# Kernel optimization log

Hardware: AMD Instinct MI355X
Metric: run time of the kernel (lower is better)

The kernel has to match this reference:

```python
import jax, jax.numpy as jnp
import numpy as np

B, L, D, DEG = 32, 1024, 512, 8
E = B * L * DEG  # 262144 edges total
N = B * L


def setup_inputs() -> dict:
    key = jax.random.key(0)
    ks = jax.random.split(key, 8)
    text_feature = jax.random.normal(ks[0], (B, L, D), jnp.float32)
    # edge list per sample (torch.nonzero(edge_matrix[i]) equivalent), offset by b*L like PyG batching
    src_local = jax.random.randint(ks[1], (E,), 0, L, jnp.int32)
    dst_local = jax.random.randint(ks[2], (E,), 0, L, jnp.int32)
    boff = (jnp.arange(E, dtype=jnp.int32) // (E // B)) * L
    edge_src = src_local + boff
    edge_dst = dst_local + boff
    s = 1.0 / np.sqrt(D)
    W1 = jax.random.uniform(ks[3], (D, D), jnp.float32, -s, s)   # node Linear
    b1 = jax.random.uniform(ks[4], (D,), jnp.float32, -s, s)
    gamma = jnp.ones((D,), jnp.float32)      # BatchNorm1d weight
    beta = jnp.zeros((D,), jnp.float32)      # BatchNorm1d bias
    run_mean = jnp.zeros((D,), jnp.float32)  # BN running stats (eval mode)
    run_var = jnp.ones((D,), jnp.float32)
    alpha1 = jnp.array(0.25, jnp.float32)    # PReLU (node MLP)
    Wg = jax.random.uniform(ks[5], (D, D), jnp.float32, -s, s)   # GCNConv lin (bias=False)
    bg = jnp.zeros((D,), jnp.float32)        # GCNConv bias
    alpha2 = jnp.array(0.25, jnp.float32)    # PReLU (after GCN)
    return {"text_feature": text_feature, "edge_src": edge_src, "edge_dst": edge_dst,
            "W1": W1, "b1": b1, "gamma": gamma, "beta": beta,
            "run_mean": run_mean, "run_var": run_var, "alpha1": alpha1,
            "Wg": Wg, "bg": bg, "alpha2": alpha2}


def reference(text_feature, edge_src, edge_dst, W1, b1, gamma, beta,
              run_mean, run_var, alpha1, Wg, bg, alpha2):
    Bs, Ls, Ds = text_feature.shape
    Nn = Bs * Ls
    xf = text_feature.reshape(Nn, Ds)
    # node MLP: Linear -> BatchNorm1d (eval) -> PReLU
    h = xf @ W1 + b1
    h = (h - run_mean) * jax.lax.rsqrt(run_var + 1e-5) * gamma + beta
    h = jnp.where(h >= 0, h, alpha1 * h)
    # GCNConv: add self loops, symmetric degree norm, gather->scatter-add, + bias
    nodes = jnp.arange(Nn, dtype=edge_src.dtype)
    src = jnp.concatenate([edge_src, nodes])
    dst = jnp.concatenate([edge_dst, nodes])
    deg = jnp.zeros((Nn,), h.dtype).at[dst].add(1.0)  # in-degree incl. self loop, >= 1
    dinv = jax.lax.rsqrt(deg)
    xw = h @ Wg                               # [N, D]
    msg = (xw * dinv[:, None])[src]           # gather D^{-1/2}-scaled messages [E+N, D]
    agg = jnp.zeros_like(xw).at[dst].add(msg) * dinv[:, None]
    g = agg + bg
    g = jnp.where(g >= 0, g, alpha2 * g)      # PReLU
    g = g.reshape(Bs, Ls, Ds)
    # F.normalize(p=2, dim=2) + residual (original input)
    g = g / jnp.clip(jnp.linalg.norm(g, axis=2, keepdims=True), 1e-12)
    return g + text_feature
```

## Files before the change

kernel.cpp:

```cpp
#include <hip/hip_runtime.h>
#include <math.h>

#define DD    512
#define NN    32768
#define EE    262144

typedef float f32x4 __attribute__((ext_vector_type(4)));
typedef __bf16 bf16x8 __attribute__((ext_vector_type(8)));

#define AS1 __attribute__((address_space(1)))
#define AS3 __attribute__((address_space(3)))

__global__ void k_zero(int* __restrict__ cnt) {
    int i = blockIdx.x * 256 + threadIdx.x;
    if (i < NN) cnt[i] = 0;
}

__global__ void k_count(const int* __restrict__ dst, int* __restrict__ cnt) {
    int e = blockIdx.x * 256 + threadIdx.x;
    if (e < EE) atomicAdd(&cnt[dst[e]], 1);
}

__global__ __launch_bounds__(1024) void k_scan(
    const int* __restrict__ cnt, int* __restrict__ offs,
    int* __restrict__ cursor, float* __restrict__ dinv)
{
    __shared__ int part[1024];
    int t = threadIdx.x;
    int base = t * 32;
    int local[32];
    int s = 0;
#pragma unroll
    for (int i = 0; i < 32; ++i) { local[i] = s; s += cnt[base + i]; }
    part[t] = s;
    __syncthreads();
    for (int off = 1; off < 1024; off <<= 1) {
        int v = (t >= off) ? part[t - off] : 0;
        __syncthreads();
        part[t] += v;
        __syncthreads();
    }
    int prev = (t == 0) ? 0 : part[t - 1];
#pragma unroll
    for (int i = 0; i < 32; ++i) {
        int o = prev + local[i];
        offs[base + i] = o;
        cursor[base + i] = o;
        dinv[base + i] = rsqrtf((float)cnt[base + i] + 1.0f);
    }
    if (t == 1023) offs[NN] = part[1023];
}

__global__ void k_fill(const int* __restrict__ src, const int* __restrict__ dst,
                       int* __restrict__ cursor, int* __restrict__ csr) {
    int e = blockIdx.x * 256 + threadIdx.x;
    if (e < EE) {
        int d = dst[e];
        int p = atomicAdd(&cursor[d], 1);
        csr[p] = src[e];
    }
}

__global__ __launch_bounds__(256) void k_wt(const float* __restrict__ W1, const float* __restrict__ Wg,
                                            __bf16* __restrict__ W1t, __bf16* __restrict__ Wgt) {
    __shared__ float tile[32][33];
    const float* W = blockIdx.z ? Wg : W1;
    __bf16* Wt = blockIdx.z ? Wgt : W1t;
    int x0 = blockIdx.x * 32;
    int y0 = blockIdx.y * 32;
    int tx = threadIdx.x;
    for (int j = threadIdx.y; j < 32; j += 8)
        tile[j][tx] = W[(size_t)(y0 + j) * DD + x0 + tx];
    __syncthreads();
    for (int j = threadIdx.y; j < 32; j += 8)
        Wt[(size_t)(x0 + j) * DD + y0 + tx] = (__bf16)tile[tx][j];
}

template <int MODE>
__global__ __launch_bounds__(512, 2) void k_gemm_w(
    const void* __restrict__ Ap,
    const __bf16* __restrict__ Wt,
    __bf16* __restrict__ Cout,
    const float* __restrict__ bias,
    const float* __restrict__ gamma, const float* __restrict__ beta,
    const float* __restrict__ mean, const float* __restrict__ var,
    const float* __restrict__ alphap)
{
    __shared__ __bf16 slab[2][32 * DD];

    const int t    = threadIdx.x;
    const int lane = t & 63;
    const int wv   = t >> 6;
    const int work = ((blockIdx.x & 7) << 5) + (blockIdx.x >> 3);
    const int nsl  = work & 1;
    const int mb   = work >> 1;
    const int mbase   = mb * 256;
    const int colbase = nsl * 256 + wv * 32;

    bf16x8 wf[2][16];
#pragma unroll
    for (int C = 0; C < 2; ++C)
#pragma unroll
        for (int kf = 0; kf < 16; ++kf) {
            int col = colbase + C * 16 + (lane & 15);
            wf[C][kf] = *(const bf16x8*)(Wt + (size_t)col * DD + kf * 32 + (lane >> 4) * 8);
        }

    float s0 = 0, s1 = 0, t0 = 0, t1 = 0, al = 0;
    if constexpr (MODE == 1) {
        int c0 = colbase + (lane & 15), c1 = c0 + 16;
        float r0 = rsqrtf(var[c0] + 1e-5f), r1 = rsqrtf(var[c1] + 1e-5f);
        s0 = gamma[c0] * r0;  s1 = gamma[c1] * r1;
        t0 = (bias[c0] - mean[c0]) * s0 + beta[c0];
        t1 = (bias[c1] - mean[c1]) * s1 + beta[c1];
        al = alphap[0];
    }

    float4 fa[4][2];

    auto loadA1 = [&](int mt) {
        const float* A = (const float*)Ap;
#pragma unroll
        for (int q = 0; q < 4; ++q) {
            int ci = q * 512 + t;
            int r = ci >> 6, c = ci & 63;
            const float* g = A + (size_t)(mbase + mt * 32 + r) * DD + c * 8;
            fa[q][0] = *(const float4*)g;
            fa[q][1] = *(const float4*)(g + 4);
        }
    };
    auto writeA1 = [&](int bb) {
#pragma unroll
        for (int q = 0; q < 4; ++q) {
            int ci = q * 512 + t;
            int r = ci >> 6, c = ci & 63;
            bf16x8 o;
            o[0] = (__bf16)fa[q][0].x; o[1] = (__bf16)fa[q][0].y;
            o[2] = (__bf16)fa[q][0].z; o[3] = (__bf16)fa[q][0].w;
            o[4] = (__bf16)fa[q][1].x; o[5] = (__bf16)fa[q][1].y;
            o[6] = (__bf16)fa[q][1].z; o[7] = (__bf16)fa[q][1].w;
            *(bf16x8*)&slab[bb][r * DD + (c ^ (r & 7)) * 8] = o;
        }
    };
    auto stage2 = [&](int bb, int mt) {
        const __bf16* A = (const __bf16*)Ap;
#pragma unroll
        for (int q = 0; q < 4; ++q) {
            int ci = q * 512 + wv * 64 + lane;
            int r = ci >> 6, c = ci & 63;
            int cl = c ^ (r & 7);
            const __bf16* g = A + (size_t)(mbase + mt * 32 + r) * DD + cl * 8;
            __builtin_amdgcn_global_load_lds(
                (const AS1 unsigned int*)g,
                (AS3 unsigned int*)(&slab[bb][(q * 512 + wv * 64) * 8]), 16, 0, 0);
        }
    };

    if constexpr (MODE == 1) { loadA1(0); writeA1(0); }
    else                     { stage2(0, 0); }
    __syncthreads();

#pragma unroll
    for (int mt = 0; mt < 8; ++mt) {
        const int cur = mt & 1, nxt = cur ^ 1;

        if (mt < 7) {
            if constexpr (MODE == 1) loadA1(mt + 1);
            else                     stage2(nxt, mt + 1);
        }

        f32x4 acc[2][2] = {};
        const __bf16* sl = &slab[cur][0];
#pragma unroll
        for (int kf = 0; kf < 16; ++kf) {
            int r0 = (lane & 15), r1 = 16 + (lane & 15);
            int c  = kf * 4 + (lane >> 4);
            bf16x8 a0 = *(const bf16x8*)&sl[r0 * DD + (c ^ (r0 & 7)) * 8];
            bf16x8 a1 = *(const bf16x8*)&sl[r1 * DD + (c ^ (r1 & 7)) * 8];
            acc[0][0] = __builtin_amdgcn_mfma_f32_16x16x32_bf16(a0, wf[0][kf], acc[0][0], 0, 0, 0);
            acc[0][1] = __builtin_amdgcn_mfma_f32_16x16x32_bf16(a0, wf[1][kf], acc[0][1], 0, 0, 0);
            acc[1][0] = __builtin_amdgcn_mfma_f32_16x16x32_bf16(a1, wf[0][kf], acc[1][0], 0, 0, 0);
            acc[1][1] = __builtin_amdgcn_mfma_f32_16x16x32_bf16(a1, wf[1][kf], acc[1][1], 0, 0, 0);
        }

#pragma unroll
        for (int R = 0; R < 2; ++R)
#pragma unroll
            for (int C = 0; C < 2; ++C) {
                int col  = colbase + C * 16 + (lane & 15);
                int rowb = mbase + mt * 32 + R * 16 + ((lane >> 4) << 2);
                float ss = C ? s1 : s0, tt = C ? t1 : t0;
#pragma unroll
                for (int j = 0; j < 4; ++j) {
                    float x = acc[R][C][j];
                    if constexpr (MODE == 1) {
                        x = x * ss + tt;
                        x = (x >= 0.0f) ? x : al * x;
                    }
                    Cout[(size_t)(rowb + j) * DD + col] = (__bf16)x;
                }
            }

        if constexpr (MODE == 1) {
            if (mt < 7) writeA1(nxt);
        }

        __syncthreads();
    }
}

__global__ __launch_bounds__(256) void k_gather_final(
    const int* __restrict__ offs, const int* __restrict__ csr,
    const __bf16* __restrict__ xws, const float* __restrict__ dinv,
    const float* __restrict__ bg, const float* __restrict__ alpha2,
    const float* __restrict__ text, float* __restrict__ out)
{
    int blk = blockIdx.x;
    int sb  = ((blk & 7) << 10) + (blk >> 3);
    int wave = threadIdx.x >> 6;
    int lane = threadIdx.x & 63;
    int node = sb * 4 + wave;
    int c = lane * 8;
    int beg = offs[node], end = offs[node + 1];
    int ne = end - beg;

    float dn = dinv[node];
    bf16x8 sv = *(const bf16x8*)(xws + (size_t)node * DD + c);
    float a[8];
#pragma unroll
    for (int i = 0; i < 8; ++i) a[i] = dn * (float)sv[i];

    int k = 0;
    for (; k + 4 <= ne; k += 4) {
        int s0 = csr[beg + k + 0];
        int s1 = csr[beg + k + 1];
        int s2 = csr[beg + k + 2];
        int s3 = csr[beg + k + 3];
        float d0 = dinv[s0], d1 = dinv[s1], d2 = dinv[s2], d3 = dinv[s3];
        bf16x8 v0 = *(const bf16x8*)(xws + (size_t)s0 * DD + c);
        bf16x8 v1 = *(const bf16x8*)(xws + (size_t)s1 * DD + c);
        bf16x8 v2 = *(const bf16x8*)(xws + (size_t)s2 * DD + c);
        bf16x8 v3 = *(const bf16x8*)(xws + (size_t)s3 * DD + c);
#pragma unroll
        for (int i = 0; i < 8; ++i)
            a[i] += d0 * (float)v0[i] + d1 * (float)v1[i] + d2 * (float)v2[i] + d3 * (float)v3[i];
    }
    for (; k < ne; ++k) {
        int s = csr[beg + k];
        float ds_ = dinv[s];
        bf16x8 v = *(const bf16x8*)(xws + (size_t)s * DD + c);
#pragma unroll
        for (int i = 0; i < 8; ++i) a[i] += ds_ * (float)v[i];
    }

    float al = alpha2[0];
    float g[8];
    float ss = 0.0f;
#pragma unroll
    for (int i = 0; i < 8; ++i) {
        float x = a[i] * dn + bg[c + i];
        x = (x >= 0.0f) ? x : al * x;
        g[i] = x;
        ss += x * x;
    }
#pragma unroll
    for (int off = 1; off < 64; off <<= 1) ss += __shfl_xor(ss, off, 64);
    float inv = 1.0f / fmaxf(sqrtf(ss), 1e-12f);

    float4 t0 = *(const float4*)(text + (size_t)node * DD + c);
    float4 t1 = *(const float4*)(text + (size_t)node * DD + c + 4);
    float4 o0, o1;
    o0.x = g[0] * inv + t0.x; o0.y = g[1] * inv + t0.y;
    o0.z = g[2] * inv + t0.z; o0.w = g[3] * inv + t0.w;
    o1.x = g[4] * inv + t1.x; o1.y = g[5] * inv + t1.y;
    o1.z = g[6] * inv + t1.z; o1.w = g[7] * inv + t1.w;
    *(float4*)(out + (size_t)node * DD + c)     = o0;
    *(float4*)(out + (size_t)node * DD + c + 4) = o1;
}

extern "C" void kernel_launch(void* const* d_in, const int* in_sizes, int n_in,
                              void* d_out, int out_size, void* d_ws, size_t ws_size,
                              hipStream_t stream) {
    const float* text   = (const float*)d_in[0];
    const int*   esrc   = (const int*)d_in[1];
    const int*   edst   = (const int*)d_in[2];
    const float* W1     = (const float*)d_in[3];
    const float* b1     = (const float*)d_in[4];
    const float* gamma  = (const float*)d_in[5];
    const float* beta   = (const float*)d_in[6];
    const float* rmean  = (const float*)d_in[7];
    const float* rvar   = (const float*)d_in[8];
    const float* alpha1 = (const float*)d_in[9];
    const float* Wg     = (const float*)d_in[10];
    const float* bg     = (const float*)d_in[11];
    const float* alpha2 = (const float*)d_in[12];
    float* out = (float*)d_out;

    char* p = (char*)d_ws;
    auto alloc = [&](size_t bytes) { char* r = p; p += (bytes + 255) & ~(size_t)255; return r; };
    int*    cnt     = (int*)alloc((size_t)NN * 4);
    int*    offs    = (int*)alloc((size_t)(NN + 1) * 4);
    int*    cursor  = (int*)alloc((size_t)NN * 4);
    float*  dinv    = (float*)alloc((size_t)NN * 4);
    int*    csr     = (int*)alloc((size_t)EE * 4);
    __bf16* W1t     = (__bf16*)alloc((size_t)DD * DD * 2);
    __bf16* Wgt     = (__bf16*)alloc((size_t)DD * DD * 2);
    __bf16* h_bf    = (__bf16*)alloc((size_t)NN * DD * 2);
    __bf16* xws     = (__bf16*)alloc((size_t)NN * DD * 2);

    k_zero<<<NN / 256, 256, 0, stream>>>(cnt);
    k_count<<<EE / 256, 256, 0, stream>>>(edst, cnt);
    k_scan<<<1, 1024, 0, stream>>>(cnt, offs, cursor, dinv);
    k_fill<<<EE / 256, 256, 0, stream>>>(esrc, edst, cursor, csr);

    k_wt<<<dim3(16, 16, 2), dim3(32, 8), 0, stream>>>(W1, Wg, W1t, Wgt);

    k_gemm_w<1><<<256, 512, 0, stream>>>(text, W1t, h_bf, b1, gamma, beta, rmean, rvar, alpha1);

    k_gemm_w<2><<<256, 512, 0, stream>>>(h_bf, Wgt, xws, nullptr, nullptr, nullptr, nullptr, nullptr, nullptr);

    k_gather_final<<<NN / 4, 256, 0, stream>>>(offs, csr, xws, dinv, bg, alpha2, text, out);
}
```

Measured before the change: 142.6 us.

## Halve GEMM row tile to 128, double grid, and use k-major LDS layout

Each GEMM block now covers 128 rows instead of 256 and the grid doubles to 512 blocks, giving better occupancy across the CUs of the GPU. The cost is that the W fragments held in registers are reloaded twice as often. The LDS slab is rearranged into a k-major layout with a new XOR swizzle on the 16-byte chunks, meant to cut bank conflicts on the MFMA fragment reads. The block-index swizzle is updated to match the new grid, and the gather kernel gets a cosmetic index cleanup.

```diff
diff --git a/kernel.cpp b/kernel.cpp
--- a/kernel.cpp
+++ b/kernel.cpp
@@ -86,15 +86,17 @@
     const float* __restrict__ mean, const float* __restrict__ var,
     const float* __restrict__ alphap)
 {
-    __shared__ __bf16 slab[2][32 * DD];
+    __shared__ __bf16 slab[2][16384];
 
     const int t    = threadIdx.x;
     const int lane = t & 63;
     const int wv   = t >> 6;
-    const int work = ((blockIdx.x & 7) << 5) + (blockIdx.x >> 3);
+    const int l15  = lane & 15;
+    const int lhi  = lane >> 4;
+    const int work = ((blockIdx.x & 7) << 6) + (blockIdx.x >> 3);
     const int nsl  = work & 1;
     const int mb   = work >> 1;
-    const int mbase   = mb * 256;
+    const int mbase   = mb * 128;
     const int colbase = nsl * 256 + wv * 32;
 
     bf16x8 wf[2][16];
@@ -102,13 +104,13 @@
     for (int C = 0; C < 2; ++C)
 #pragma unroll
         for (int kf = 0; kf < 16; ++kf) {
-            int col = colbase + C * 16 + (lane & 15);
-            wf[C][kf] = *(const bf16x8*)(Wt + (size_t)col * DD + kf * 32 + (lane >> 4) * 8);
+            int col = colbase + C * 16 + l15;
+            wf[C][kf] = *(const bf16x8*)(Wt + (size_t)col * DD + kf * 32 + lhi * 8);
         }
 
     float s0 = 0, s1 = 0, t0 = 0, t1 = 0, al = 0;
     if constexpr (MODE == 1) {
-        int c0 = colbase + (lane & 15), c1 = c0 + 16;
+        int c0 = colbase + l15, c1 = c0 + 16;
         float r0 = rsqrtf(var[c0] + 1e-5f), r1 = rsqrtf(var[c1] + 1e-5f);
         s0 = gamma[c0] * r0;  s1 = gamma[c1] * r1;
         t0 = (bias[c0] - mean[c0]) * s0 + beta[c0];
@@ -122,8 +124,9 @@
         const float* A = (const float*)Ap;
 #pragma unroll
         for (int q = 0; q < 4; ++q) {
-            int ci = q * 512 + t;
-            int r = ci >> 6, c = ci & 63;
+            int d = q * 512 + t;
+            int kf = d >> 7, r = (d >> 2) & 31, s = d & 3;
+            int c = kf * 4 + (s ^ ((r >> 1) & 3));
             const float* g = A + (size_t)(mbase + mt * 32 + r) * DD + c * 8;
             fa[q][0] = *(const float4*)g;
             fa[q][1] = *(const float4*)(g + 4);
@@ -132,27 +135,26 @@
     auto writeA1 = [&](int bb) {
 #pragma unroll
         for (int q = 0; q < 4; ++q) {
-            int ci = q * 512 + t;
-            int r = ci >> 6, c = ci & 63;
+            int d = q * 512 + t;
             bf16x8 o;
             o[0] = (__bf16)fa[q][0].x; o[1] = (__bf16)fa[q][0].y;
             o[2] = (__bf16)fa[q][0].z; o[3] = (__bf16)fa[q][0].w;
             o[4] = (__bf16)fa[q][1].x; o[5] = (__bf16)fa[q][1].y;
             o[6] = (__bf16)fa[q][1].z; o[7] = (__bf16)fa[q][1].w;
-            *(bf16x8*)&slab[bb][r * DD + (c ^ (r & 7)) * 8] = o;
+            *(bf16x8*)&slab[bb][(size_t)d * 8] = o;
         }
     };
     auto stage2 = [&](int bb, int mt) {
         const __bf16* A = (const __bf16*)Ap;
 #pragma unroll
         for (int q = 0; q < 4; ++q) {
-            int ci = q * 512 + wv * 64 + lane;
-            int r = ci >> 6, c = ci & 63;
-            int cl = c ^ (r & 7);
-            const __bf16* g = A + (size_t)(mbase + mt * 32 + r) * DD + cl * 8;
+            int d  = q * 512 + wv * 64 + lane;
+            int kf = d >> 7, r = (d >> 2) & 31, s = d & 3;
+            int c  = kf * 4 + (s ^ ((r >> 1) & 3));
+            const __bf16* g = A + (size_t)(mbase + mt * 32 + r) * DD + c * 8;
             __builtin_amdgcn_global_load_lds(
                 (const AS1 unsigned int*)g,
-                (AS3 unsigned int*)(&slab[bb][(q * 512 + wv * 64) * 8]), 16, 0, 0);
+                (AS3 unsigned int*)(&slab[bb][(size_t)(q * 512 + wv * 64) * 8]), 16, 0, 0);
         }
     };
 
@@ -161,10 +163,10 @@
     __syncthreads();
 
 #pragma unroll
-    for (int mt = 0; mt < 8; ++mt) {
+    for (int mt = 0; mt < 4; ++mt) {
         const int cur = mt & 1, nxt = cur ^ 1;
 
-        if (mt < 7) {
+        if (mt < 3) {
             if constexpr (MODE == 1) loadA1(mt + 1);
             else                     stage2(nxt, mt + 1);
         }
@@ -173,10 +175,11 @@
         const __bf16* sl = &slab[cur][0];
 #pragma unroll
         for (int kf = 0; kf < 16; ++kf) {
-            int r0 = (lane & 15), r1 = 16 + (lane & 15);
-            int c  = kf * 4 + (lane >> 4);
-            bf16x8 a0 = *(const bf16x8*)&sl[r0 * DD + (c ^ (r0 & 7)) * 8];
-            bf16x8 a1 = *(const bf16x8*)&sl[r1 * DD + (c ^ (r1 & 7)) * 8];
+            int r0 = l15, r1 = 16 + l15;
+            int sA = lhi ^ ((r0 >> 1) & 3);
+            int sB = lhi ^ ((r1 >> 1) & 3);
+            bf16x8 a0 = *(const bf16x8*)&sl[(kf * 128 + r0 * 4 + sA) * 8];
+            bf16x8 a1 = *(const bf16x8*)&sl[(kf * 128 + r1 * 4 + sB) * 8];
             acc[0][0] = __builtin_amdgcn_mfma_f32_16x16x32_bf16(a0, wf[0][kf], acc[0][0], 0, 0, 0);
             acc[0][1] = __builtin_amdgcn_mfma_f32_16x16x32_bf16(a0, wf[1][kf], acc[0][1], 0, 0, 0);
             acc[1][0] = __builtin_amdgcn_mfma_f32_16x16x32_bf16(a1, wf[0][kf], acc[1][0], 0, 0, 0);
@@ -187,13 +190,13 @@
         for (int R = 0; R < 2; ++R)
 #pragma unroll
             for (int C = 0; C < 2; ++C) {
-                int col  = colbase + C * 16 + (lane & 15);
-                int rowb = mbase + mt * 32 + R * 16 + ((lane >> 4) << 2);
-                float ss = C ? s1 : s0, tt = C ? t1 : t0;
+                int col  = colbase + C * 16 + l15;
+                int rowb = mbase + mt * 32 + R * 16 + (lhi << 2);
 #pragma unroll
                 for (int j = 0; j < 4; ++j) {
                     float x = acc[R][C][j];
                     if constexpr (MODE == 1) {
+                        float ss = C ? s1 : s0, tt = C ? t1 : t0;
                         x = x * ss + tt;
                         x = (x >= 0.0f) ? x : al * x;
                     }
@@ -202,7 +205,7 @@
             }
 
         if constexpr (MODE == 1) {
-            if (mt < 7) writeA1(nxt);
+            if (mt < 3) writeA1(nxt);
         }
 
         __syncthreads();
@@ -267,15 +270,16 @@
     for (int off = 1; off < 64; off <<= 1) ss += __shfl_xor(ss, off, 64);
     float inv = 1.0f / fmaxf(sqrtf(ss), 1e-12f);
 
-    float4 t0 = *(const float4*)(text + (size_t)node * DD + c);
-    float4 t1 = *(const float4*)(text + (size_t)node * DD + c + 4);
+    size_t base = (size_t)node * DD + c;
+    float4 t0 = *(const float4*)&text[base];
+    float4 t1 = *(const float4*)&text[base + 4];
     float4 o0, o1;
     o0.x = g[0] * inv + t0.x; o0.y = g[1] * inv + t0.y;
     o0.z = g[2] * inv + t0.z; o0.w = g[3] * inv + t0.w;
     o1.x = g[4] * inv + t1.x; o1.y = g[5] * inv + t1.y;
     o1.z = g[6] * inv + t1.z; o1.w = g[7] * inv + t1.w;
-    *(float4*)(out + (size_t)node * DD + c)     = o0;
-    *(float4*)(out + (size_t)node * DD + c + 4) = o1;
+    *(float4*)&out[base]     = o0;
+    *(float4*)&out[base + 4] = o1;
 }
 
 extern "C" void kernel_launch(void* const* d_in, const int* in_sizes, int n_in,
@@ -315,9 +319,9 @@
 
     k_wt<<<dim3(16, 16, 2), dim3(32, 8), 0, stream>>>(W1, Wg, W1t, Wgt);
 
-    k_gemm_w<1><<<256, 512, 0, stream>>>(text, W1t, h_bf, b1, gamma, beta, rmean, rvar, alpha1);
-
-    k_gemm_w<2><<<256, 512, 0, stream>>>(h_bf, Wgt, xws, nullptr, nullptr, nullptr, nullptr, nullptr, nullptr);
+    k_gemm_w<1><<<512, 512, 0, stream>>>(text, W1t, h_bf, b1, gamma, beta, rmean, rvar, alpha1);
+
+    k_gemm_w<2><<<512, 512, 0, stream>>>(h_bf, Wgt, xws, nullptr, nullptr, nullptr, nullptr, nullptr, nullptr);
 
     k_gather_final<<<NN / 4, 256, 0, stream>>>(offs, csr, xws, dinv, bg, alpha2, text, out);
 }
```

Measured after the change: 158.3 us. 1.11x slower.
